# Performance work log

Hardware: AMD Instinct MI355X
Metric: run time of the kernel (lower is better)

The kernel has to match this reference:

```python
import jax, jax.numpy as jnp
import numpy as np

N_EMBD = 384
NUM_HEADS = 6
HEAD_SIZE = 64
B, T = 64, 256


def setup_inputs() -> dict:
    key = jax.random.key(0)
    ks = jax.random.split(key, 6)
    s = 0.02
    x = jax.random.normal(ks[0], (B, T, N_EMBD), dtype=jnp.float32)
    # per-head projection weights, stored as [H, in, out] so y = x @ W
    Wq = jax.random.normal(ks[1], (NUM_HEADS, N_EMBD, HEAD_SIZE), dtype=jnp.float32) * s
    Wk = jax.random.normal(ks[2], (NUM_HEADS, N_EMBD, HEAD_SIZE), dtype=jnp.float32) * s
    Wv = jax.random.normal(ks[3], (NUM_HEADS, N_EMBD, HEAD_SIZE), dtype=jnp.float32) * s
    Wp = jax.random.normal(ks[4], (NUM_HEADS * HEAD_SIZE, N_EMBD), dtype=jnp.float32) * s
    bp = jax.random.normal(ks[5], (N_EMBD,), dtype=jnp.float32) * s
    return {"x": x, "Wq": Wq, "Wk": Wk, "Wv": Wv, "Wp": Wp, "bp": bp}


def reference(x, Wq, Wk, Wv, Wp, bp):
    # x: [B,T,C]; W{q,k,v}: [H,C,D]; dropout is identity (eval mode)
    Bb, Tt, _ = x.shape
    q = jnp.einsum('btc,hcd->bhtd', x, Wq)
    k = jnp.einsum('btc,hcd->bhtd', x, Wk)
    v = jnp.einsum('btc,hcd->bhtd', x, Wv)
    scale = HEAD_SIZE ** -0.5
    scores = jnp.einsum('bhtd,bhsd->bhts', q, k) * scale  # [B,H,T,T]
    causal = jnp.tril(jnp.ones((Tt, Tt), dtype=bool))
    scores = jnp.where(causal, scores, jnp.finfo(scores.dtype).min)
    attn = jax.nn.softmax(scores, axis=-1)
    out = jnp.einsum('bhts,bhsd->bhtd', attn, v)  # [B,H,T,D]
    out = out.transpose(0, 2, 1, 3).reshape(Bb, Tt, NUM_HEADS * HEAD_SIZE)
    return out @ Wp + bp
```

## Files before the change

kernel.cpp:

```cpp
#include <hip/hip_runtime.h>
#include <stdint.h>

#define B_  64
#define T_  256
#define C_  384
#define H_  6
#define D_  64
#define NTOK (B_*T_)

typedef float f32x4 __attribute__((ext_vector_type(4)));
typedef short s16x8 __attribute__((ext_vector_type(8)));

__device__ __forceinline__ unsigned short f2bf(float f) {
    unsigned int u;
    __builtin_memcpy(&u, &f, 4);
    u = u + 0x7FFFu + ((u >> 16) & 1u);
    return (unsigned short)(u >> 16);
}

__device__ __forceinline__ void async_copy16(const unsigned short* g, unsigned short* l) {
    __builtin_amdgcn_global_load_lds(
        (const __attribute__((address_space(1))) unsigned int*)g,
        (__attribute__((address_space(3))) unsigned int*)l, 16, 0, 0);
}

__global__ __launch_bounds__(256) void convert_x(
    const float* __restrict__ x, unsigned short* __restrict__ xb) {
    int i = (blockIdx.x * 256 + threadIdx.x) * 4;
    float4 v = *reinterpret_cast<const float4*>(x + i);
    ushort4 o;
    o.x = f2bf(v.x); o.y = f2bf(v.y); o.z = f2bf(v.z); o.w = f2bf(v.w);
    *reinterpret_cast<ushort4*>(xb + i) = o;
}

__global__ __launch_bounds__(256) void transpose_weights(
    const float* __restrict__ Wq, const float* __restrict__ Wk,
    const float* __restrict__ Wv, const float* __restrict__ Wp,
    unsigned short* __restrict__ WTq, unsigned short* __restrict__ WTk,
    unsigned short* __restrict__ WTv, unsigned short* __restrict__ WTp) {
    __shared__ float tile[32][33];
    int z = blockIdx.y;
    const float* in;
    unsigned short* out;
    int R, Cc;
    if (z < 18) {
        int proj = z / 6, h = z % 6;
        const float* Wsrc = proj == 0 ? Wq : (proj == 1 ? Wk : Wv);
        unsigned short* Wdst = proj == 0 ? WTq : (proj == 1 ? WTk : WTv);
        in = Wsrc + h * C_ * D_;
        out = Wdst + h * C_ * D_;
        R = C_; Cc = D_;
    } else {
        in = Wp; out = WTp; R = C_; Cc = C_;
    }
    int tilesC = Cc / 32;
    int tilesR = R / 32;
    int bx = blockIdx.x;
    if (bx >= tilesC * tilesR) return;
    int tr = bx / tilesC, tc = bx % tilesC;
    int tx = threadIdx.x & 31;
    int ty8 = threadIdx.x >> 5;
    int gx = tc * 32 + tx;
#pragma unroll
    for (int i = 0; i < 4; i++) {
        int gy = tr * 32 + ty8 + i * 8;
        tile[ty8 + i * 8][tx] = in[gy * Cc + gx];
    }
    __syncthreads();
#pragma unroll
    for (int i = 0; i < 4; i++) {
        int oy = tc * 32 + ty8 + i * 8;
        int ox = tr * 32 + tx;
        out[oy * R + ox] = f2bf(tile[tx][ty8 + i * 8]);
    }
}

__global__ __launch_bounds__(256) void gemm_qkv(
    const unsigned short* __restrict__ Xb,
    const unsigned short* __restrict__ WT,
    unsigned short* __restrict__ qws, unsigned short* __restrict__ kws,
    unsigned short* __restrict__ vTws) {
    __shared__ alignas(16) unsigned short Bt[6 * 128 * 32];
    int m0 = blockIdx.x * 128;
    int y = blockIdx.y;
    int n0 = y * 128;
    int tid = threadIdx.x;
    int w = tid >> 6, lane = tid & 63;
    int n16 = lane & 15, q4 = lane >> 4;

    f32x4 acc[2][8];
#pragma unroll
    for (int i = 0; i < 2; i++)
#pragma unroll
        for (int j = 0; j < 8; j++) acc[i][j] = (f32x4){0.f, 0.f, 0.f, 0.f};

    const unsigned short* a_base[2];
#pragma unroll
    for (int mi = 0; mi < 2; mi++)
        a_base[mi] = Xb + (size_t)(m0 + w * 32 + mi * 16 + n16) * C_ + q4 * 8;

    bool swapped = (y < 6);
    for (int half = 0; half < 2; half++) {
        int ko = half * 192;
        s16x8 af[2][6];
#pragma unroll
        for (int mi = 0; mi < 2; mi++)
#pragma unroll
            for (int ks = 0; ks < 6; ks++)
                af[mi][ks] = *reinterpret_cast<const s16x8*>(a_base[mi] + ko + ks * 32);
        if (half) __syncthreads();
#pragma unroll
        for (int i = 0; i < 12; i++) {
            int L = w * 768 + i * 64 + lane;
            int kstep = L >> 9;
            int rem = L & 511;
            int row = rem >> 2;
            int j = (rem & 3) ^ (row & 3);
            async_copy16(WT + (size_t)(n0 + row) * C_ + ko + kstep * 32 + j * 8,
                         Bt + (size_t)(w * 768 + i * 64) * 8);
        }
        __syncthreads();
#pragma unroll
        for (int ks = 0; ks < 6; ks++) {
            s16x8 bf[8];
#pragma unroll
            for (int ni = 0; ni < 8; ni++) {
                int row = ni * 16 + n16;
                int jp = q4 ^ (row & 3);
                bf[ni] = *reinterpret_cast<const s16x8*>(&Bt[ks * 4096 + row * 32 + jp * 8]);
            }
            if (swapped) {
#pragma unroll
                for (int mi = 0; mi < 2; mi++)
#pragma unroll
                    for (int ni = 0; ni < 8; ni++)
                        acc[mi][ni] = __builtin_amdgcn_mfma_f32_16x16x32_bf16(
                            bf[ni], af[mi][ks], acc[mi][ni], 0, 0, 0);
            } else {
#pragma unroll
                for (int mi = 0; mi < 2; mi++)
#pragma unroll
                    for (int ni = 0; ni < 8; ni++)
                        acc[mi][ni] = __builtin_amdgcn_mfma_f32_16x16x32_bf16(
                            af[mi][ks], bf[ni], acc[mi][ni], 0, 0, 0);
            }
        }
    }

    if (swapped) {
        unsigned short* outp = (y < 3) ? qws : kws;
        int n0w = (y % 3) * 128;
#pragma unroll
        for (int mi = 0; mi < 2; mi++) {
            int tr = m0 + w * 32 + mi * 16 + n16;
#pragma unroll
            for (int ni = 0; ni < 8; ni++) {
                int c0 = n0w + ni * 16 + q4 * 4;
                ushort4 pk;
                pk.x = f2bf(acc[mi][ni][0]); pk.y = f2bf(acc[mi][ni][1]);
                pk.z = f2bf(acc[mi][ni][2]); pk.w = f2bf(acc[mi][ni][3]);
                *reinterpret_cast<ushort4*>(&outp[(size_t)tr * C_ + c0]) = pk;
            }
        }
    } else {
        int n0w = (y - 6) * 128;
#pragma unroll
        for (int mi = 0; mi < 2; mi++) {
            int t4 = m0 + w * 32 + mi * 16 + q4 * 4;
            int b = t4 >> 8, t = t4 & 255;
#pragma unroll
            for (int ni = 0; ni < 8; ni++) {
                int c = n0w + ni * 16 + n16;
                int h = c >> 6, d = c & 63;
                ushort4 pk;
                pk.x = f2bf(acc[mi][ni][0]); pk.y = f2bf(acc[mi][ni][1]);
                pk.z = f2bf(acc[mi][ni][2]); pk.w = f2bf(acc[mi][ni][3]);
                *reinterpret_cast<ushort4*>(&vTws[((size_t)(b * H_ + h) * D_ + d) * T_ + t]) = pk;
            }
        }
    }
}

__global__ __launch_bounds__(256) void attn_fwd(
    const unsigned short* qws, const unsigned short* __restrict__ kws,
    const unsigned short* __restrict__ vTws, unsigned short* Ows) {
    __shared__ alignas(16) unsigned short Kt[256 * 64];
    __shared__ alignas(16) unsigned short Vt[64 * 256];
    __shared__ alignas(16) unsigned short p_lds[4][2][16 * 40];
    int z = blockIdx.x;
    int bh = blockIdx.y;
    int b = bh / H_, h = bh % H_;
    int tid = threadIdx.x;
    int w = tid >> 6, lane = tid & 63;
    int n16 = lane & 15, q4 = lane >> 4;

#pragma unroll
    for (int i = 0; i < 8; i++) {
        int L = w * 512 + i * 64 + lane;
        int r = L >> 3;
        int j = (L & 7) ^ (r & 7);
        async_copy16(kws + (size_t)(b * T_ + r) * C_ + h * 64 + j * 8,
                     Kt + (size_t)(w * 512 + i * 64) * 8);
    }
#pragma unroll
    for (int i = 0; i < 8; i++) {
        int L = w * 512 + i * 64 + lane;
        int d = L >> 5;
        int j = (L & 31) ^ (d & 7);
        async_copy16(vTws + ((size_t)bh * 64 + d) * T_ + j * 8,
                     Vt + (size_t)(w * 512 + i * 64) * 8);
    }
    __syncthreads();

    const f32x4 zero4 = (f32x4){0.f, 0.f, 0.f, 0.f};
    int p = z * 4 + w;

#pragma unroll
    for (int tt = 0; tt < 2; tt++) {
        int j = (tt == 0) ? p : 15 - p;
        int t0 = j * 16;

        const unsigned short* qbase =
            qws + (size_t)(b * T_ + t0 + n16) * C_ + h * 64 + q4 * 8;
        s16x8 qa0 = *reinterpret_cast<const s16x8*>(qbase);
        s16x8 qa1 = *reinterpret_cast<const s16x8*>(qbase + 32);

        f32x4 o[4];
        float l_lane[4];
#pragma unroll
        for (int i = 0; i < 4; i++) o[i] = zero4;
#pragma unroll
        for (int r = 0; r < 4; r++) l_lane[r] = 0.f;

        int nch = j / 2 + 1;
#pragma unroll 2
        for (int c = 0; c < nch; c++) {
            int s0 = c * 32;
            bool bAct = (s0 + 16) < (t0 + 16);
            int r0 = s0 + n16, r1 = s0 + 16 + n16;
            s16x8 k00 = *reinterpret_cast<const s16x8*>(&Kt[r0 * 64 + ((q4 ^ (r0 & 7)) * 8)]);
            s16x8 k01 = *reinterpret_cast<const s16x8*>(&Kt[r0 * 64 + (((q4 + 4) ^ (r0 & 7)) * 8)]);
            f32x4 sv0 = __builtin_amdgcn_mfma_f32_16x16x32_bf16(qa0, k00, zero4, 0, 0, 0);
            sv0 = __builtin_amdgcn_mfma_f32_16x16x32_bf16(qa1, k01, sv0, 0, 0, 0);
            f32x4 sv1 = zero4;
            if (bAct) {
                s16x8 k10 = *reinterpret_cast<const s16x8*>(&Kt[r1 * 64 + ((q4 ^ (r1 & 7)) * 8)]);
                s16x8 k11 = *reinterpret_cast<const s16x8*>(&Kt[r1 * 64 + (((q4 + 4) ^ (r1 & 7)) * 8)]);
                sv1 = __builtin_amdgcn_mfma_f32_16x16x32_bf16(qa0, k10, zero4, 0, 0, 0);
                sv1 = __builtin_amdgcn_mfma_f32_16x16x32_bf16(qa1, k11, sv1, 0, 0, 0);
            }
            unsigned short* pw = &p_lds[w][c & 1][0];
#pragma unroll
            for (int r = 0; r < 4; r++) {
                int t = t0 + q4 * 4 + r;
                float pA = (s0 + n16 <= t) ? __expf(sv0[r] * 0.125f) : 0.f;
                float pB = (bAct && (s0 + 16 + n16 <= t)) ? __expf(sv1[r] * 0.125f) : 0.f;
                l_lane[r] += pA + pB;
                pw[(q4 * 4 + r) * 40 + n16] = f2bf(pA);
                pw[(q4 * 4 + r) * 40 + 16 + n16] = f2bf(pB);
            }
            s16x8 pa = *reinterpret_cast<const s16x8*>(&pw[n16 * 40 + q4 * 8]);
#pragma unroll
            for (int dt = 0; dt < 4; dt++) {
                int d = dt * 16 + n16;
                int jp = (c * 4 + q4) ^ (d & 7);
                s16x8 vf = *reinterpret_cast<const s16x8*>(&Vt[d * 256 + jp * 8]);
                o[dt] = __builtin_amdgcn_mfma_f32_16x16x32_bf16(pa, vf, o[dt], 0, 0, 0);
            }
        }

        float linv[4];
#pragma unroll
        for (int r = 0; r < 4; r++) {
            float l = l_lane[r];
            l += __shfl_xor(l, 1);
            l += __shfl_xor(l, 2);
            l += __shfl_xor(l, 4);
            l += __shfl_xor(l, 8);
            linv[r] = 1.0f / l;
        }
#pragma unroll
        for (int dt = 0; dt < 4; dt++) {
            int col = h * 64 + dt * 16 + n16;
#pragma unroll
            for (int r = 0; r < 4; r++)
                Ows[(size_t)(b * T_ + t0 + q4 * 4 + r) * C_ + col] = f2bf(o[dt][r] * linv[r]);
        }
    }
}

__global__ __launch_bounds__(256) void gemm_out(
    const unsigned short* __restrict__ A, const unsigned short* __restrict__ WTp,
    const float* __restrict__ bp, float* __restrict__ out) {
    __shared__ alignas(16) unsigned short Bt[6 * 128 * 32];
    int m0 = blockIdx.x * 128;
    int n0 = blockIdx.y * 128;
    int tid = threadIdx.x;
    int w = tid >> 6, lane = tid & 63;
    int n16 = lane & 15, q4 = lane >> 4;

    f32x4 acc[2][8];
#pragma unroll
    for (int i = 0; i < 2; i++)
#pragma unroll
        for (int j = 0; j < 8; j++) acc[i][j] = (f32x4){0.f, 0.f, 0.f, 0.f};

    const unsigned short* a_base[2];
#pragma unroll
    for (int mi = 0; mi < 2; mi++)
        a_base[mi] = A + (size_t)(m0 + w * 32 + mi * 16 + n16) * C_ + q4 * 8;

    for (int half = 0; half < 2; half++) {
        int ko = half * 192;
        s16x8 af[2][6];
#pragma unroll
        for (int mi = 0; mi < 2; mi++)
#pragma unroll
            for (int ks = 0; ks < 6; ks++)
                af[mi][ks] = *reinterpret_cast<const s16x8*>(a_base[mi] + ko + ks * 32);
        if (half) __syncthreads();
#pragma unroll
        for (int i = 0; i < 12; i++) {
            int L = w * 768 + i * 64 + lane;
            int kstep = L >> 9;
            int rem = L & 511;
            int row = rem >> 2;
            int j = (rem & 3) ^ (row & 3);
            async_copy16(WTp + (size_t)(n0 + row) * C_ + ko + kstep * 32 + j * 8,
                         Bt + (size_t)(w * 768 + i * 64) * 8);
        }
        __syncthreads();
#pragma unroll
        for (int ks = 0; ks < 6; ks++) {
            s16x8 bf[8];
#pragma unroll
            for (int ni = 0; ni < 8; ni++) {
                int row = ni * 16 + n16;
                int jp = q4 ^ (row & 3);
                bf[ni] = *reinterpret_cast<const s16x8*>(&Bt[ks * 4096 + row * 32 + jp * 8]);
            }
#pragma unroll
            for (int mi = 0; mi < 2; mi++)
#pragma unroll
                for (int ni = 0; ni < 8; ni++)
                    acc[mi][ni] = __builtin_amdgcn_mfma_f32_16x16x32_bf16(
                        bf[ni], af[mi][ks], acc[mi][ni], 0, 0, 0);
        }
    }

#pragma unroll
    for (int mi = 0; mi < 2; mi++) {
        int tr = m0 + w * 32 + mi * 16 + n16;
#pragma unroll
        for (int ni = 0; ni < 8; ni++) {
            int c0 = n0 + ni * 16 + q4 * 4;
            float4 bias = *reinterpret_cast<const float4*>(&bp[c0]);
            float4 res;
            res.x = acc[mi][ni][0] + bias.x;
            res.y = acc[mi][ni][1] + bias.y;
            res.z = acc[mi][ni][2] + bias.z;
            res.w = acc[mi][ni][3] + bias.w;
            *reinterpret_cast<float4*>(&out[(size_t)tr * C_ + c0]) = res;
        }
    }
}

extern "C" void kernel_launch(void* const* d_in, const int* in_sizes, int n_in,
                              void* d_out, int out_size, void* d_ws, size_t ws_size,
                              hipStream_t stream) {
    const float* x  = (const float*)d_in[0];
    const float* Wq = (const float*)d_in[1];
    const float* Wk = (const float*)d_in[2];
    const float* Wv = (const float*)d_in[3];
    const float* Wp = (const float*)d_in[4];
    const float* bp = (const float*)d_in[5];
    float* out = (float*)d_out;

    char* ws = (char*)d_ws;
    size_t off = 0;
    auto alloc = [&](size_t bytes) -> unsigned short* {
        unsigned short* p = (unsigned short*)(ws + off);
        off += (bytes + 255) & ~(size_t)255;
        return p;
    };
    unsigned short* WTq = alloc((size_t)H_ * C_ * D_ * 2);
    unsigned short* WTk = alloc((size_t)H_ * C_ * D_ * 2);
    unsigned short* WTv = alloc((size_t)H_ * C_ * D_ * 2);
    unsigned short* WTp = alloc((size_t)C_ * C_ * 2);
    unsigned short* xb  = alloc((size_t)NTOK * C_ * 2);
    unsigned short* qws = alloc((size_t)NTOK * C_ * 2);
    unsigned short* kws = alloc((size_t)NTOK * C_ * 2);
    unsigned short* vTw = alloc((size_t)NTOK * C_ * 2);
    unsigned short* Ows = qws;

    convert_x<<<dim3(NTOK * C_ / 4 / 256), dim3(256), 0, stream>>>(x, xb);
    transpose_weights<<<dim3(144, 19), dim3(256), 0, stream>>>(
        Wq, Wk, Wv, Wp, WTq, WTk, WTv, WTp);
    gemm_qkv<<<dim3(128, 9), dim3(256), 0, stream>>>(
        xb, WTq, qws, kws, vTw);
    attn_fwd<<<dim3(2, B_ * H_), dim3(256), 0, stream>>>(
        qws, kws, vTw, Ows);
    gemm_out<<<dim3(128, 3), dim3(256), 0, stream>>>(
        Ows, WTp, bp, out);
}
```

Measured before the change: 172.9 us.

## Fuse QKV projection into attention kernel per batch-head, keeping Q/K/V in LDS

Replaces the separate x conversion, QKV GEMM and attention kernels with one fused kernel per (batch, head). Each block reads fp32 x directly, converts it to bf16 in registers, projects it against an interleaved per-head QKV weight block, and writes Q, K and V^T straight into LDS for the causal attention. This removes the global round trips for the bf16 copy of x and for the Q/K/V intermediates, plus two kernel launches. In exchange, each head's block re-reads its batch's x, so x is read six times. The grid is 384 blocks of 512 threads using about 135 KB of LDS per block, which could limit occupancy.

```diff
diff --git a/kernel.cpp b/kernel.cpp
--- a/kernel.cpp
+++ b/kernel.cpp
@@ -24,20 +24,10 @@
         (__attribute__((address_space(3))) unsigned int*)l, 16, 0, 0);
 }
 
-__global__ __launch_bounds__(256) void convert_x(
-    const float* __restrict__ x, unsigned short* __restrict__ xb) {
-    int i = (blockIdx.x * 256 + threadIdx.x) * 4;
-    float4 v = *reinterpret_cast<const float4*>(x + i);
-    ushort4 o;
-    o.x = f2bf(v.x); o.y = f2bf(v.y); o.z = f2bf(v.z); o.w = f2bf(v.w);
-    *reinterpret_cast<ushort4*>(xb + i) = o;
-}
-
 __global__ __launch_bounds__(256) void transpose_weights(
     const float* __restrict__ Wq, const float* __restrict__ Wk,
     const float* __restrict__ Wv, const float* __restrict__ Wp,
-    unsigned short* __restrict__ WTq, unsigned short* __restrict__ WTk,
-    unsigned short* __restrict__ WTv, unsigned short* __restrict__ WTp) {
+    unsigned short* __restrict__ W3, unsigned short* __restrict__ WTp) {
     __shared__ float tile[32][33];
     int z = blockIdx.y;
     const float* in;
@@ -46,9 +36,8 @@
     if (z < 18) {
         int proj = z / 6, h = z % 6;
         const float* Wsrc = proj == 0 ? Wq : (proj == 1 ? Wk : Wv);
-        unsigned short* Wdst = proj == 0 ? WTq : (proj == 1 ? WTk : WTv);
         in = Wsrc + h * C_ * D_;
-        out = Wdst + h * C_ * D_;
+        out = W3 + (size_t)(h * 192 + proj * 64) * C_;
         R = C_; Cc = D_;
     } else {
         in = Wp; out = WTp; R = C_; Cc = C_;
@@ -75,155 +64,117 @@
     }
 }
 
-__global__ __launch_bounds__(256) void gemm_qkv(
-    const unsigned short* __restrict__ Xb,
-    const unsigned short* __restrict__ WT,
-    unsigned short* __restrict__ qws, unsigned short* __restrict__ kws,
-    unsigned short* __restrict__ vTws) {
-    __shared__ alignas(16) unsigned short Bt[6 * 128 * 32];
-    int m0 = blockIdx.x * 128;
-    int y = blockIdx.y;
-    int n0 = y * 128;
+__global__ __launch_bounds__(512, 2) void fused_attn(
+    const float* __restrict__ X, const unsigned short* __restrict__ W3,
+    unsigned short* __restrict__ Ows) {
+    __shared__ alignas(16) unsigned short smem[67584];
+    unsigned short* Wc     = smem;
+    unsigned short* q_lds  = smem + 18432;
+    unsigned short* k_lds  = q_lds + 16384;
+    unsigned short* vT_lds = k_lds + 16384;
+
+    int bh = blockIdx.x;
+    int h = bh >> 6, b = bh & 63;
     int tid = threadIdx.x;
     int w = tid >> 6, lane = tid & 63;
     int n16 = lane & 15, q4 = lane >> 4;
-
-    f32x4 acc[2][8];
+    const int jt[2] = {w, 15 - w};
+
+    const unsigned short* W3h = W3 + (size_t)h * 192 * C_;
+    const float* xb = X + (size_t)b * T_ * C_;
+
+    f32x4 acc[2][12];
 #pragma unroll
     for (int i = 0; i < 2; i++)
 #pragma unroll
-        for (int j = 0; j < 8; j++) acc[i][j] = (f32x4){0.f, 0.f, 0.f, 0.f};
-
-    const unsigned short* a_base[2];
-#pragma unroll
-    for (int mi = 0; mi < 2; mi++)
-        a_base[mi] = Xb + (size_t)(m0 + w * 32 + mi * 16 + n16) * C_ + q4 * 8;
-
-    bool swapped = (y < 6);
-    for (int half = 0; half < 2; half++) {
-        int ko = half * 192;
-        s16x8 af[2][6];
+        for (int j = 0; j < 12; j++) acc[i][j] = (f32x4){0.f, 0.f, 0.f, 0.f};
+
+    for (int kc = 0; kc < 4; kc++) {
+        int ko = kc * 96;
+        float4 a0[2][3], a1[2][3];
 #pragma unroll
         for (int mi = 0; mi < 2; mi++)
 #pragma unroll
-            for (int ks = 0; ks < 6; ks++)
-                af[mi][ks] = *reinterpret_cast<const s16x8*>(a_base[mi] + ko + ks * 32);
-        if (half) __syncthreads();
-#pragma unroll
-        for (int i = 0; i < 12; i++) {
-            int L = w * 768 + i * 64 + lane;
-            int kstep = L >> 9;
-            int rem = L & 511;
-            int row = rem >> 2;
-            int j = (rem & 3) ^ (row & 3);
-            async_copy16(WT + (size_t)(n0 + row) * C_ + ko + kstep * 32 + j * 8,
-                         Bt + (size_t)(w * 768 + i * 64) * 8);
+            for (int ks = 0; ks < 3; ks++) {
+                const float* ap = xb + (size_t)(jt[mi] * 16 + n16) * C_ + ko + ks * 32 + q4 * 8;
+                a0[mi][ks] = *reinterpret_cast<const float4*>(ap);
+                a1[mi][ks] = *reinterpret_cast<const float4*>(ap + 4);
+            }
+        if (kc) __syncthreads();
+#pragma unroll
+        for (int i = 0; i < 5; i++) {
+            int sb = i * 512 + w * 64;
+            if (sb < 2304) {
+                int L = sb + lane;
+                int row = L / 12;
+                int c = L % 12;
+                int ks = c >> 2;
+                int q4g = (c & 3) ^ (row & 3);
+                async_copy16(W3h + (size_t)row * C_ + ko + ks * 32 + q4g * 8,
+                             Wc + (size_t)sb * 8);
+            }
         }
         __syncthreads();
 #pragma unroll
-        for (int ks = 0; ks < 6; ks++) {
-            s16x8 bf[8];
-#pragma unroll
-            for (int ni = 0; ni < 8; ni++) {
+        for (int ks = 0; ks < 3; ks++) {
+            s16x8 af[2];
+#pragma unroll
+            for (int mi = 0; mi < 2; mi++) {
+                float4 lo = a0[mi][ks], hi = a1[mi][ks];
+                s16x8 a;
+                a[0] = (short)f2bf(lo.x); a[1] = (short)f2bf(lo.y);
+                a[2] = (short)f2bf(lo.z); a[3] = (short)f2bf(lo.w);
+                a[4] = (short)f2bf(hi.x); a[5] = (short)f2bf(hi.y);
+                a[6] = (short)f2bf(hi.z); a[7] = (short)f2bf(hi.w);
+                af[mi] = a;
+            }
+#pragma unroll
+            for (int ni = 0; ni < 12; ni++) {
                 int row = ni * 16 + n16;
-                int jp = q4 ^ (row & 3);
-                bf[ni] = *reinterpret_cast<const s16x8*>(&Bt[ks * 4096 + row * 32 + jp * 8]);
-            }
-            if (swapped) {
-#pragma unroll
-                for (int mi = 0; mi < 2; mi++)
-#pragma unroll
-                    for (int ni = 0; ni < 8; ni++)
-                        acc[mi][ni] = __builtin_amdgcn_mfma_f32_16x16x32_bf16(
-                            bf[ni], af[mi][ks], acc[mi][ni], 0, 0, 0);
+                int cp = ks * 4 + (q4 ^ (row & 3));
+                s16x8 bf = *reinterpret_cast<const s16x8*>(&Wc[row * 96 + cp * 8]);
+                if (ni < 8) {
+                    acc[0][ni] = __builtin_amdgcn_mfma_f32_16x16x32_bf16(bf, af[0], acc[0][ni], 0, 0, 0);
+                    acc[1][ni] = __builtin_amdgcn_mfma_f32_16x16x32_bf16(bf, af[1], acc[1][ni], 0, 0, 0);
+                } else {
+                    acc[0][ni] = __builtin_amdgcn_mfma_f32_16x16x32_bf16(af[0], bf, acc[0][ni], 0, 0, 0);
+                    acc[1][ni] = __builtin_amdgcn_mfma_f32_16x16x32_bf16(af[1], bf, acc[1][ni], 0, 0, 0);
+                }
+            }
+        }
+    }
+#pragma unroll
+    for (int mi = 0; mi < 2; mi++) {
+        int tile = jt[mi];
+#pragma unroll
+        for (int ni = 0; ni < 12; ni++) {
+            ushort4 pk;
+            pk.x = f2bf(acc[mi][ni][0]); pk.y = f2bf(acc[mi][ni][1]);
+            pk.z = f2bf(acc[mi][ni][2]); pk.w = f2bf(acc[mi][ni][3]);
+            if (ni < 8) {
+                int t = tile * 16 + n16;
+                int cp = (2 * (ni & 3) + (q4 >> 1)) ^ (n16 & 7);
+                unsigned short* dst = (ni < 4) ? q_lds : k_lds;
+                *reinterpret_cast<ushort4*>(&dst[t * 64 + cp * 8 + (q4 & 1) * 4]) = pk;
             } else {
-#pragma unroll
-                for (int mi = 0; mi < 2; mi++)
-#pragma unroll
-                    for (int ni = 0; ni < 8; ni++)
-                        acc[mi][ni] = __builtin_amdgcn_mfma_f32_16x16x32_bf16(
-                            af[mi][ks], bf[ni], acc[mi][ni], 0, 0, 0);
-            }
-        }
-    }
-
-    if (swapped) {
-        unsigned short* outp = (y < 3) ? qws : kws;
-        int n0w = (y % 3) * 128;
-#pragma unroll
-        for (int mi = 0; mi < 2; mi++) {
-            int tr = m0 + w * 32 + mi * 16 + n16;
-#pragma unroll
-            for (int ni = 0; ni < 8; ni++) {
-                int c0 = n0w + ni * 16 + q4 * 4;
-                ushort4 pk;
-                pk.x = f2bf(acc[mi][ni][0]); pk.y = f2bf(acc[mi][ni][1]);
-                pk.z = f2bf(acc[mi][ni][2]); pk.w = f2bf(acc[mi][ni][3]);
-                *reinterpret_cast<ushort4*>(&outp[(size_t)tr * C_ + c0]) = pk;
-            }
-        }
-    } else {
-        int n0w = (y - 6) * 128;
-#pragma unroll
-        for (int mi = 0; mi < 2; mi++) {
-            int t4 = m0 + w * 32 + mi * 16 + q4 * 4;
-            int b = t4 >> 8, t = t4 & 255;
-#pragma unroll
-            for (int ni = 0; ni < 8; ni++) {
-                int c = n0w + ni * 16 + n16;
-                int h = c >> 6, d = c & 63;
-                ushort4 pk;
-                pk.x = f2bf(acc[mi][ni][0]); pk.y = f2bf(acc[mi][ni][1]);
-                pk.z = f2bf(acc[mi][ni][2]); pk.w = f2bf(acc[mi][ni][3]);
-                *reinterpret_cast<ushort4*>(&vTws[((size_t)(b * H_ + h) * D_ + d) * T_ + t]) = pk;
-            }
-        }
-    }
-}
-
-__global__ __launch_bounds__(256) void attn_fwd(
-    const unsigned short* qws, const unsigned short* __restrict__ kws,
-    const unsigned short* __restrict__ vTws, unsigned short* Ows) {
-    __shared__ alignas(16) unsigned short Kt[256 * 64];
-    __shared__ alignas(16) unsigned short Vt[64 * 256];
-    __shared__ alignas(16) unsigned short p_lds[4][2][16 * 40];
-    int z = blockIdx.x;
-    int bh = blockIdx.y;
-    int b = bh / H_, h = bh % H_;
-    int tid = threadIdx.x;
-    int w = tid >> 6, lane = tid & 63;
-    int n16 = lane & 15, q4 = lane >> 4;
-
-#pragma unroll
-    for (int i = 0; i < 8; i++) {
-        int L = w * 512 + i * 64 + lane;
-        int r = L >> 3;
-        int j = (L & 7) ^ (r & 7);
-        async_copy16(kws + (size_t)(b * T_ + r) * C_ + h * 64 + j * 8,
-                     Kt + (size_t)(w * 512 + i * 64) * 8);
-    }
-#pragma unroll
-    for (int i = 0; i < 8; i++) {
-        int L = w * 512 + i * 64 + lane;
-        int d = L >> 5;
-        int j = (L & 31) ^ (d & 7);
-        async_copy16(vTws + ((size_t)bh * 64 + d) * T_ + j * 8,
-                     Vt + (size_t)(w * 512 + i * 64) * 8);
+                int d = (ni - 8) * 16 + n16;
+                int cp = (tile * 2 + (q4 >> 1)) ^ (d & 7);
+                *reinterpret_cast<ushort4*>(&vT_lds[d * 256 + cp * 8 + (q4 & 1) * 4]) = pk;
+            }
+        }
     }
     __syncthreads();
 
+    unsigned short* pw_base = smem + w * 1280;
     const f32x4 zero4 = (f32x4){0.f, 0.f, 0.f, 0.f};
-    int p = z * 4 + w;
 
 #pragma unroll
     for (int tt = 0; tt < 2; tt++) {
-        int j = (tt == 0) ? p : 15 - p;
+        int j = jt[tt];
         int t0 = j * 16;
-
-        const unsigned short* qbase =
-            qws + (size_t)(b * T_ + t0 + n16) * C_ + h * 64 + q4 * 8;
-        s16x8 qa0 = *reinterpret_cast<const s16x8*>(qbase);
-        s16x8 qa1 = *reinterpret_cast<const s16x8*>(qbase + 32);
+        int tq = t0 + n16;
+        s16x8 qa0 = *reinterpret_cast<const s16x8*>(&q_lds[tq * 64 + ((q4 ^ (n16 & 7)) * 8)]);
+        s16x8 qa1 = *reinterpret_cast<const s16x8*>(&q_lds[tq * 64 + (((q4 + 4) ^ (n16 & 7)) * 8)]);
 
         f32x4 o[4];
         float l_lane[4];
@@ -233,23 +184,22 @@
         for (int r = 0; r < 4; r++) l_lane[r] = 0.f;
 
         int nch = j / 2 + 1;
-#pragma unroll 2
         for (int c = 0; c < nch; c++) {
             int s0 = c * 32;
             bool bAct = (s0 + 16) < (t0 + 16);
             int r0 = s0 + n16, r1 = s0 + 16 + n16;
-            s16x8 k00 = *reinterpret_cast<const s16x8*>(&Kt[r0 * 64 + ((q4 ^ (r0 & 7)) * 8)]);
-            s16x8 k01 = *reinterpret_cast<const s16x8*>(&Kt[r0 * 64 + (((q4 + 4) ^ (r0 & 7)) * 8)]);
+            s16x8 k00 = *reinterpret_cast<const s16x8*>(&k_lds[r0 * 64 + ((q4 ^ (r0 & 7)) * 8)]);
+            s16x8 k01 = *reinterpret_cast<const s16x8*>(&k_lds[r0 * 64 + (((q4 + 4) ^ (r0 & 7)) * 8)]);
             f32x4 sv0 = __builtin_amdgcn_mfma_f32_16x16x32_bf16(qa0, k00, zero4, 0, 0, 0);
             sv0 = __builtin_amdgcn_mfma_f32_16x16x32_bf16(qa1, k01, sv0, 0, 0, 0);
             f32x4 sv1 = zero4;
             if (bAct) {
-                s16x8 k10 = *reinterpret_cast<const s16x8*>(&Kt[r1 * 64 + ((q4 ^ (r1 & 7)) * 8)]);
-                s16x8 k11 = *reinterpret_cast<const s16x8*>(&Kt[r1 * 64 + (((q4 + 4) ^ (r1 & 7)) * 8)]);
+                s16x8 k10 = *reinterpret_cast<const s16x8*>(&k_lds[r1 * 64 + ((q4 ^ (r1 & 7)) * 8)]);
+                s16x8 k11 = *reinterpret_cast<const s16x8*>(&k_lds[r1 * 64 + (((q4 + 4) ^ (r1 & 7)) * 8)]);
                 sv1 = __builtin_amdgcn_mfma_f32_16x16x32_bf16(qa0, k10, zero4, 0, 0, 0);
                 sv1 = __builtin_amdgcn_mfma_f32_16x16x32_bf16(qa1, k11, sv1, 0, 0, 0);
             }
-            unsigned short* pw = &p_lds[w][c & 1][0];
+            unsigned short* pw = pw_base + (c & 1) * 640;
 #pragma unroll
             for (int r = 0; r < 4; r++) {
                 int t = t0 + q4 * 4 + r;
@@ -264,7 +214,7 @@
             for (int dt = 0; dt < 4; dt++) {
                 int d = dt * 16 + n16;
                 int jp = (c * 4 + q4) ^ (d & 7);
-                s16x8 vf = *reinterpret_cast<const s16x8*>(&Vt[d * 256 + jp * 8]);
+                s16x8 vf = *reinterpret_cast<const s16x8*>(&vT_lds[d * 256 + jp * 8]);
                 o[dt] = __builtin_amdgcn_mfma_f32_16x16x32_bf16(pa, vf, o[dt], 0, 0, 0);
             }
         }
@@ -383,23 +333,12 @@
         off += (bytes + 255) & ~(size_t)255;
         return p;
     };
-    unsigned short* WTq = alloc((size_t)H_ * C_ * D_ * 2);
-    unsigned short* WTk = alloc((size_t)H_ * C_ * D_ * 2);
-    unsigned short* WTv = alloc((size_t)H_ * C_ * D_ * 2);
+    unsigned short* W3  = alloc((size_t)H_ * 192 * C_ * 2);
     unsigned short* WTp = alloc((size_t)C_ * C_ * 2);
-    unsigned short* xb  = alloc((size_t)NTOK * C_ * 2);
-    unsigned short* qws = alloc((size_t)NTOK * C_ * 2);
-    unsigned short* kws = alloc((size_t)NTOK * C_ * 2);
-    unsigned short* vTw = alloc((size_t)NTOK * C_ * 2);
-    unsigned short* Ows = qws;
-
-    convert_x<<<dim3(NTOK * C_ / 4 / 256), dim3(256), 0, stream>>>(x, xb);
+    unsigned short* Ows = alloc((size_t)NTOK * C_ * 2);
+
     transpose_weights<<<dim3(144, 19), dim3(256), 0, stream>>>(
-        Wq, Wk, Wv, Wp, WTq, WTk, WTv, WTp);
-    gemm_qkv<<<dim3(128, 9), dim3(256), 0, stream>>>(
-        xb, WTq, qws, kws, vTw);
-    attn_fwd<<<dim3(2, B_ * H_), dim3(256), 0, stream>>>(
-        qws, kws, vTw, Ows);
-    gemm_out<<<dim3(128, 3), dim3(256), 0, stream>>>(
-        Ows, WTp, bp, out);
-}
+        Wq, Wk, Wv, Wp, W3, WTp);
+    fused_attn<<<dim3(B_ * H_), dim3(512), 0, stream>>>(x, W3, Ows);
+    gemm_out<<<dim3(128, 3), dim3(256), 0, stream>>>(Ows, WTp, bp, out);
+}
```

Result: faster. 151.3 us (-12.5%).
